# Kernel tuning notes

Measured on AMD Instinct MI355X. Metric: run time of the kernel, lower is better.

Reference implementation:

```python
import jax, jax.numpy as jnp
import numpy as np

B, N, NID, V, GH, PHI, RHO = 8, 256, 64, 128, 128, 256, 128
BN = B * N
EPS = 1e-5


def _layernorm(x, g, b):
    m = jnp.mean(x, axis=-1, keepdims=True)
    v = jnp.var(x, axis=-1, keepdims=True)
    return (x - m) * jax.lax.rsqrt(v + EPS) * g + b


def _edges(A):
    # dense adjacency -> flat batched edge list, exactly as mask.nonzero() ordering
    bidx = jnp.arange(B)[:, None, None]
    ii = jnp.arange(N)[None, :, None]
    jj = jnp.arange(N)[None, None, :]
    src = jnp.broadcast_to(bidx * N + ii, (B, N, N)).reshape(-1)  # edge_index[0] = b*N+i
    tgt = jnp.broadcast_to(bidx * N + jj, (B, N, N)).reshape(-1)  # edge_index[1] = b*N+j
    w = A.reshape(-1)
    valid = w != 0
    rel = (w > 0).astype(jnp.int32)
    return src, tgt, w, valid, rel


def _rgcn(H, src, tgt, valid, rel, Wrel, Wroot, bias):
    # torch_geometric RGCNConv: mean aggregation per relation at target + root + bias
    x_src = H[src]  # (E, d) gather
    out = H @ Wroot + bias
    for r in range(2):
        m = (valid & (rel == r)).astype(H.dtype)  # (E,)
        s = jax.ops.segment_sum(x_src * m[:, None], tgt, num_segments=BN)
        c = jax.ops.segment_sum(m, tgt, num_segments=BN)
        out = out + (s / jnp.maximum(c, 1.0)[:, None]) @ Wrel[r]
    return out


def setup_inputs() -> dict:
    key = jax.random.key(0)
    ks = jax.random.split(key, 24)
    p = lambda k, shape: jax.random.normal(k, shape, dtype=jnp.float32) * 0.02
    z = lambda *shape: jnp.zeros(shape, jnp.float32)
    return {
        "A": jax.random.normal(ks[0], (B, N, N), dtype=jnp.float32),
        "X": jax.random.normal(ks[1], (B, N, NID), dtype=jnp.float32),
        "home_mask": (jax.random.uniform(ks[2], (B, N)) > 0.5).astype(jnp.float32),
        "emb1_w": p(ks[3], (NID, V)), "emb1_b": z(V),
        "emb2_w": p(ks[4], (V, V)), "emb2_b": z(V),
        "rgcn_w_0": p(ks[5], (2, V, GH)), "rgcn_root_0": p(ks[6], (V, GH)), "rgcn_bias_0": z(GH),
        "lina_w_0": p(ks[7], (GH, GH)), "lina_b_0": z(GH),
        "linb_w_0": p(ks[8], (GH, GH)), "linb_b_0": z(GH),
        "rgcn_w_1": p(ks[9], (2, GH, GH)), "rgcn_root_1": p(ks[10], (GH, GH)), "rgcn_bias_1": z(GH),
        "lina_w_1": p(ks[11], (GH, GH)), "lina_b_1": z(GH),
        "linb_w_1": p(ks[12], (GH, GH)), "linb_b_1": z(GH),
        "norm_g": jnp.ones((GH,), jnp.float32), "norm_b": z(GH),
        "phi_w1": p(ks[13], (GH, PHI)), "phi_b1": z(PHI),
        "phi_w2": p(ks[14], (PHI, PHI)), "phi_b2": z(PHI),
        "rho_w1": p(ks[15], (PHI, RHO)), "rho_b1": z(RHO),
        "rho_w2": p(ks[16], (RHO, 1)), "rho_b2": z(1),
    }


def reference(A, X, home_mask, emb1_w, emb1_b, emb2_w, emb2_b,
              rgcn_w_0, rgcn_root_0, rgcn_bias_0, lina_w_0, lina_b_0, linb_w_0, linb_b_0,
              rgcn_w_1, rgcn_root_1, rgcn_bias_1, lina_w_1, lina_b_1, linb_w_1, linb_b_1,
              norm_g, norm_b, phi_w1, phi_b1, phi_w2, phi_b2,
              rho_w1, rho_b1, rho_w2, rho_b2):
    away_mask = 1.0 - home_mask
    H = jax.nn.relu(X @ emb1_w + emb1_b)
    H = (H @ emb2_w + emb2_b).reshape(BN, V)

    src, tgt, w, valid, rel = _edges(A)
    aw = jnp.abs(w) * valid.astype(w.dtype)  # |edge_weight|, zero for masked-out edges

    blocks = [
        (rgcn_w_0, rgcn_root_0, rgcn_bias_0, lina_w_0, lina_b_0, linb_w_0, linb_b_0),
        (rgcn_w_1, rgcn_root_1, rgcn_bias_1, lina_w_1, lina_b_1, linb_w_1, linb_b_1),
    ]
    agg = jnp.zeros_like(H)
    for (Wrel, Wroot, bias, law, lab, lbw, lbb) in blocks:
        H = H + agg
        H2 = _rgcn(H, src, tgt, valid, rel, Wrel, Wroot, bias)
        # gather-scale-scatter: agg[src] += H2[tgt] * |w|
        agg = jax.ops.segment_sum(H2[tgt] * aw[:, None], src, num_segments=BN)
        agg = jax.nn.relu(_layernorm(agg, norm_g, norm_b))  # dropout = identity (eval)
        agg = jax.nn.relu(agg @ law + lab)
        agg = agg @ lbw + lbb
    H = (H + agg).reshape(B, N, GH)

    # DeepSet phi (dropout = identity)
    h = jax.nn.relu(H @ phi_w1 + phi_b1)
    phi_out = jax.nn.relu(h @ phi_w2 + phi_b2)  # (B, N, PHI)

    home_sum = jnp.sum(phi_out * home_mask[:, :, None], axis=1)
    away_sum = jnp.sum(phi_out * away_mask[:, :, None], axis=1)

    def rho(s):
        return (jax.nn.relu(s @ rho_w1 + rho_b1) @ rho_w2 + rho_b2)[:, 0]

    out = rho(home_sum) - rho(away_sum)
    return 0.5 + 0.5 * jnp.tanh(out)  # (B,)
```

## Files before the change

kernel.cpp:

```cpp
#include <hip/hip_runtime.h>
#include <math.h>

#define NB 8


__global__ __launch_bounds__(512, 2) void k_embed(const float* __restrict__ X,
        const float* __restrict__ w1, const float* __restrict__ b1,
        const float* __restrict__ w2, const float* __restrict__ b2,
        float* __restrict__ H, float* __restrict__ pools) {
    const int r0 = blockIdx.x * 8;
    const int t = threadIdx.x, q = t & 31, u = t >> 5, w = t >> 6;
    __shared__ __align__(16) float part[8192];
    __shared__ __align__(16) float xq[512];
    __shared__ __align__(16) float h1q[1024];
    if (blockIdx.x < 8) pools[blockIdx.x * 512 + t] = 0.f;
    {
        int r = t >> 6, k = t & 63;
        xq[k * 8 + r] = X[(size_t)(r0 + r) * 64 + k];
    }
    __syncthreads();
    {
        float acc[32];
        #pragma unroll
        for (int i = 0; i < 32; ++i) acc[i] = 0.f;
        #pragma unroll
        for (int kk = 0; kk < 4; ++kk) {
            int k = u * 4 + kk;
            float4 w4 = *(const float4*)&w1[(size_t)k * 128 + q * 4];
            float wc[4] = {w4.x, w4.y, w4.z, w4.w};
            float4 xa = *(const float4*)&xq[k * 8];
            float4 xb = *(const float4*)&xq[k * 8 + 4];
            float xr[8] = {xa.x, xa.y, xa.z, xa.w, xb.x, xb.y, xb.z, xb.w};
            #pragma unroll
            for (int r = 0; r < 8; ++r)
                #pragma unroll
                for (int c = 0; c < 4; ++c)
                    acc[r * 4 + c] = fmaf(xr[r], wc[c], acc[r * 4 + c]);
        }
        #pragma unroll
        for (int i = 0; i < 32; ++i) acc[i] += __shfl_down(acc[i], 32, 64);
        if ((t & 63) < 32)
            #pragma unroll
            for (int r = 0; r < 8; ++r)
                *(float4*)&part[w * 1024 + r * 128 + q * 4] =
                    make_float4(acc[r*4+0], acc[r*4+1], acc[r*4+2], acc[r*4+3]);
    }
    __syncthreads();
    #pragma unroll
    for (int e = 0; e < 2; ++e) {
        int idx = e * 512 + t;
        int r = idx >> 7, f = idx & 127;
        float s = b1[f];
        #pragma unroll
        for (int uu = 0; uu < 8; ++uu) s += part[uu * 1024 + r * 128 + f];
        h1q[f * 8 + r] = fmaxf(s, 0.f);
    }
    __syncthreads();
    {
        float acc[32];
        #pragma unroll
        for (int i = 0; i < 32; ++i) acc[i] = 0.f;
        #pragma unroll
        for (int kk = 0; kk < 8; ++kk) {
            int k = u * 8 + kk;
            float4 w4 = *(const float4*)&w2[(size_t)k * 128 + q * 4];
            float wc[4] = {w4.x, w4.y, w4.z, w4.w};
            float4 xa = *(const float4*)&h1q[k * 8];
            float4 xb = *(const float4*)&h1q[k * 8 + 4];
            float xr[8] = {xa.x, xa.y, xa.z, xa.w, xb.x, xb.y, xb.z, xb.w};
            #pragma unroll
            for (int r = 0; r < 8; ++r)
                #pragma unroll
                for (int c = 0; c < 4; ++c)
                    acc[r * 4 + c] = fmaf(xr[r], wc[c], acc[r * 4 + c]);
        }
        #pragma unroll
        for (int i = 0; i < 32; ++i) acc[i] += __shfl_down(acc[i], 32, 64);
        if ((t & 63) < 32)
            #pragma unroll
            for (int r = 0; r < 8; ++r)
                *(float4*)&part[w * 1024 + r * 128 + q * 4] =
                    make_float4(acc[r*4+0], acc[r*4+1], acc[r*4+2], acc[r*4+3]);
    }
    __syncthreads();
    #pragma unroll
    for (int e = 0; e < 2; ++e) {
        int idx = e * 512 + t;
        int r = idx >> 7, f = idx & 127;
        float s = b2[f];
        #pragma unroll
        for (int uu = 0; uu < 8; ++uu) s += part[uu * 1024 + r * 128 + f];
        H[(size_t)(r0 + r) * 128 + f] = s;
    }
}

__global__ __launch_bounds__(512, 2) void k_gcn1(
        const float* __restrict__ A, const float* __restrict__ H,
        const float* __restrict__ Wrel, const float* __restrict__ Wroot,
        const float* __restrict__ bias, float* __restrict__ H2) {
    const int b  = blockIdx.x >> 5;
    const int j0 = (blockIdx.x & 31) * 8;
    const int t = threadIdx.x, q = t & 31, u = t >> 5, w = t >> 6;
    __shared__ __align__(16) float maskM[4096];
    __shared__ __align__(16) float part[8192];
    __shared__ __align__(16) float pb[3072];
    __shared__ float cntp[512];
    __shared__ float cnt[16];
    const float* Ab = A + (size_t)b * 65536;
    const float* Hb = H + (size_t)b * 32768;
    const float* W0 = Wrel;
    const float* W1 = Wrel + 16384;

    if (t < 256) {
        float4 a0 = *(const float4*)(Ab + (size_t)t * 256 + j0);
        float4 a1 = *(const float4*)(Ab + (size_t)t * 256 + j0 + 4);
        float av[8] = {a0.x, a0.y, a0.z, a0.w, a1.x, a1.y, a1.z, a1.w};
        #pragma unroll
        for (int j = 0; j < 8; ++j) {
            maskM[t * 16 + j]     = (av[j] < 0.f) ? 1.f : 0.f;
            maskM[t * 16 + 8 + j] = (av[j] > 0.f) ? 1.f : 0.f;
        }
    }
    __syncthreads();
    {
        int chunk = t >> 4, slot = t & 15;
        float c = 0.f;
        #pragma unroll
        for (int qq = 0; qq < 8; ++qq) c += maskM[(chunk * 8 + qq) * 16 + slot];
        cntp[slot * 32 + chunk] = c;
    }
    __syncthreads();
    if (t < 16) {
        float s = 0.f;
        #pragma unroll
        for (int c = 0; c < 32; ++c) s += cntp[t * 32 + c];
        cnt[t] = s;
    }
    {
        float acc[32];
        #pragma unroll
        for (int i = 0; i < 32; ++i) acc[i] = 0.f;
        #pragma unroll 8
        for (int ii = 0; ii < 16; ++ii) {
            int i = u * 16 + ii;
            float4 h4 = *(const float4*)&Hb[(size_t)i * 128 + q * 4];
            float hc[4] = {h4.x, h4.y, h4.z, h4.w};
            float4 ma = *(const float4*)&maskM[i * 16];
            float4 mb = *(const float4*)&maskM[i * 16 + 4];
            float mr[8] = {ma.x, ma.y, ma.z, ma.w, mb.x, mb.y, mb.z, mb.w};
            #pragma unroll
            for (int r = 0; r < 8; ++r)
                #pragma unroll
                for (int c = 0; c < 4; ++c)
                    acc[r * 4 + c] = fmaf(mr[r], hc[c], acc[r * 4 + c]);
        }
        #pragma unroll
        for (int i = 0; i < 32; ++i) acc[i] += __shfl_down(acc[i], 32, 64);
        if ((t & 63) < 32)
            #pragma unroll
            for (int r = 0; r < 8; ++r)
                *(float4*)&part[w * 1024 + r * 128 + q * 4] =
                    make_float4(acc[r*4+0], acc[r*4+1], acc[r*4+2], acc[r*4+3]);
    }
    __syncthreads();
    #pragma unroll
    for (int e = 0; e < 2; ++e) {
        int idx = e * 512 + t;
        int r = idx >> 7, f = idx & 127;
        float s = 0.f;
        #pragma unroll
        for (int uu = 0; uu < 8; ++uu) s += part[uu * 1024 + r * 128 + f];
        pb[f * 24 + 8 + r] = s * (1.f / fmaxf(cnt[r], 1.f));
    }
    __syncthreads();
    {
        float acc[32];
        #pragma unroll
        for (int i = 0; i < 32; ++i) acc[i] = 0.f;
        #pragma unroll 8
        for (int ii = 0; ii < 16; ++ii) {
            int i = u * 16 + ii;
            float4 h4 = *(const float4*)&Hb[(size_t)i * 128 + q * 4];
            float hc[4] = {h4.x, h4.y, h4.z, h4.w};
            float4 ma = *(const float4*)&maskM[i * 16 + 8];
            float4 mb = *(const float4*)&maskM[i * 16 + 12];
            float mr[8] = {ma.x, ma.y, ma.z, ma.w, mb.x, mb.y, mb.z, mb.w};
            #pragma unroll
            for (int r = 0; r < 8; ++r)
                #pragma unroll
                for (int c = 0; c < 4; ++c)
                    acc[r * 4 + c] = fmaf(mr[r], hc[c], acc[r * 4 + c]);
        }
        #pragma unroll
        for (int i = 0; i < 32; ++i) acc[i] += __shfl_down(acc[i], 32, 64);
        if ((t & 63) < 32)
            #pragma unroll
            for (int r = 0; r < 8; ++r)
                *(float4*)&part[w * 1024 + r * 128 + q * 4] =
                    make_float4(acc[r*4+0], acc[r*4+1], acc[r*4+2], acc[r*4+3]);
    }
    __syncthreads();
    #pragma unroll
    for (int e = 0; e < 2; ++e) {
        int idx = e * 512 + t;
        int r = idx >> 7, f = idx & 127;
        float s = 0.f;
        #pragma unroll
        for (int uu = 0; uu < 8; ++uu) s += part[uu * 1024 + r * 128 + f];
        pb[f * 24 + 16 + r] = s * (1.f / fmaxf(cnt[8 + r], 1.f));
        pb[f * 24 + r] = Hb[(size_t)(j0 + r) * 128 + f];
    }
    __syncthreads();
    {
        float acc[32];
        #pragma unroll
        for (int i = 0; i < 32; ++i) acc[i] = 0.f;
        #pragma unroll 4
        for (int kk = 0; kk < 8; ++kk) {
            int k = u * 8 + kk;
            float4 wr = *(const float4*)&Wroot[(size_t)k * 128 + q * 4];
            float4 wa = *(const float4*)&W0[(size_t)k * 128 + q * 4];
            float4 wb = *(const float4*)&W1[(size_t)k * 128 + q * 4];
            float wrc[4] = {wr.x, wr.y, wr.z, wr.w};
            float wac[4] = {wa.x, wa.y, wa.z, wa.w};
            float wbc[4] = {wb.x, wb.y, wb.z, wb.w};
            float4 h0 = *(const float4*)&pb[k * 24];
            float4 h1 = *(const float4*)&pb[k * 24 + 4];
            float4 p0 = *(const float4*)&pb[k * 24 + 8];
            float4 p1 = *(const float4*)&pb[k * 24 + 12];
            float4 q0 = *(const float4*)&pb[k * 24 + 16];
            float4 q1 = *(const float4*)&pb[k * 24 + 20];
            float hr[8]  = {h0.x, h0.y, h0.z, h0.w, h1.x, h1.y, h1.z, h1.w};
            float m0r[8] = {p0.x, p0.y, p0.z, p0.w, p1.x, p1.y, p1.z, p1.w};
            float m1r[8] = {q0.x, q0.y, q0.z, q0.w, q1.x, q1.y, q1.z, q1.w};
            #pragma unroll
            for (int r = 0; r < 8; ++r)
                #pragma unroll
                for (int c = 0; c < 4; ++c) {
                    float v = acc[r * 4 + c];
                    v = fmaf(hr[r],  wrc[c], v);
                    v = fmaf(m0r[r], wac[c], v);
                    v = fmaf(m1r[r], wbc[c], v);
                    acc[r * 4 + c] = v;
                }
        }
        #pragma unroll
        for (int i = 0; i < 32; ++i) acc[i] += __shfl_down(acc[i], 32, 64);
        if ((t & 63) < 32)
            #pragma unroll
            for (int r = 0; r < 8; ++r)
                *(float4*)&part[w * 1024 + r * 128 + q * 4] =
                    make_float4(acc[r*4+0], acc[r*4+1], acc[r*4+2], acc[r*4+3]);
    }
    __syncthreads();
    #pragma unroll
    for (int e = 0; e < 2; ++e) {
        int idx = e * 512 + t;
        int r = idx >> 7, f = idx & 127;
        float s = bias[f];
        #pragma unroll
        for (int uu = 0; uu < 8; ++uu) s += part[uu * 1024 + r * 128 + f];
        H2[(size_t)(b * 256 + j0 + r) * 128 + f] = s;
    }
}

__global__ __launch_bounds__(512, 2) void k_gcn2(
        const float* __restrict__ A, const float* __restrict__ H2,
        const float* __restrict__ g, const float* __restrict__ bta,
        const float* __restrict__ law, const float* __restrict__ lab,
        const float* __restrict__ lbw, const float* __restrict__ lbb,
        float* __restrict__ H) {
    const int b  = blockIdx.x >> 5;
    const int i0 = (blockIdx.x & 31) * 8;
    const int t = threadIdx.x, q = t & 31, u = t >> 5, w = t >> 6;
    __shared__ __align__(16) float part[8192];
    __shared__ __align__(16) float absA[2048];
    __shared__ __align__(16) float xq[1024];
    __shared__ __align__(16) float uq[1024];
    __shared__ float red[32];
    __shared__ float mi[16];
    const float* Ab  = A + (size_t)b * 65536;
    const float* H2b = H2 + (size_t)b * 32768;

    if (t < 256) {
        #pragma unroll
        for (int r = 0; r < 8; ++r)
            absA[t * 8 + r] = fabsf(Ab[(size_t)(i0 + r) * 256 + t]);
    }
    __syncthreads();
    {
        float acc[32];
        #pragma unroll
        for (int i = 0; i < 32; ++i) acc[i] = 0.f;
        #pragma unroll 8
        for (int jj = 0; jj < 16; ++jj) {
            int j = u * 16 + jj;
            float4 h4 = *(const float4*)&H2b[(size_t)j * 128 + q * 4];
            float hc[4] = {h4.x, h4.y, h4.z, h4.w};
            float4 aa = *(const float4*)&absA[j * 8];
            float4 ab = *(const float4*)&absA[j * 8 + 4];
            float ar[8] = {aa.x, aa.y, aa.z, aa.w, ab.x, ab.y, ab.z, ab.w};
            #pragma unroll
            for (int r = 0; r < 8; ++r)
                #pragma unroll
                for (int c = 0; c < 4; ++c)
                    acc[r * 4 + c] = fmaf(ar[r], hc[c], acc[r * 4 + c]);
        }
        #pragma unroll
        for (int i = 0; i < 32; ++i) acc[i] += __shfl_down(acc[i], 32, 64);
        if ((t & 63) < 32)
            #pragma unroll
            for (int r = 0; r < 8; ++r)
                *(float4*)&part[w * 1024 + r * 128 + q * 4] =
                    make_float4(acc[r*4+0], acc[r*4+1], acc[r*4+2], acc[r*4+3]);
    }
    __syncthreads();
    float xv[2];
    const int fof = t & 127;
    #pragma unroll
    for (int e = 0; e < 2; ++e) {
        int idx = e * 512 + t;
        int r = idx >> 7;
        float s = 0.f;
        #pragma unroll
        for (int uu = 0; uu < 8; ++uu) s += part[uu * 1024 + r * 128 + fof];
        xv[e] = s;
        float sw = s, s2 = s * s;
        #pragma unroll
        for (int o = 32; o > 0; o >>= 1) {
            sw += __shfl_down(sw, o, 64);
            s2 += __shfl_down(s2, o, 64);
        }
        if ((t & 63) == 0) {
            int half = (t >> 6) & 1;
            red[r * 4 + half * 2]     = sw;
            red[r * 4 + half * 2 + 1] = s2;
        }
    }
    __syncthreads();
    if (t < 8) {
        float s  = red[t * 4]     + red[t * 4 + 2];
        float s2 = red[t * 4 + 1] + red[t * 4 + 3];
        float m = s * (1.f / 128.f);
        float v = s2 * (1.f / 128.f) - m * m;
        mi[t * 2] = m;
        mi[t * 2 + 1] = rsqrtf(v + 1e-5f);
    }
    __syncthreads();
    {
        float gf = g[fof], bf = bta[fof];
        #pragma unroll
        for (int e = 0; e < 2; ++e) {
            int r = ((e * 512 + t) >> 7);
            xq[fof * 8 + r] = fmaxf((xv[e] - mi[r * 2]) * mi[r * 2 + 1] * gf + bf, 0.f);
        }
    }
    __syncthreads();
    {
        float acc[32];
        #pragma unroll
        for (int i = 0; i < 32; ++i) acc[i] = 0.f;
        #pragma unroll
        for (int kk = 0; kk < 8; ++kk) {
            int k = u * 8 + kk;
            float4 w4 = *(const float4*)&law[(size_t)k * 128 + q * 4];
            float wc[4] = {w4.x, w4.y, w4.z, w4.w};
            float4 xa = *(const float4*)&xq[k * 8];
            float4 xb = *(const float4*)&xq[k * 8 + 4];
            float xr[8] = {xa.x, xa.y, xa.z, xa.w, xb.x, xb.y, xb.z, xb.w};
            #pragma unroll
            for (int r = 0; r < 8; ++r)
                #pragma unroll
                for (int c = 0; c < 4; ++c)
                    acc[r * 4 + c] = fmaf(xr[r], wc[c], acc[r * 4 + c]);
        }
        #pragma unroll
        for (int i = 0; i < 32; ++i) acc[i] += __shfl_down(acc[i], 32, 64);
        if ((t & 63) < 32)
            #pragma unroll
            for (int r = 0; r < 8; ++r)
                *(float4*)&part[w * 1024 + r * 128 + q * 4] =
                    make_float4(acc[r*4+0], acc[r*4+1], acc[r*4+2], acc[r*4+3]);
    }
    __syncthreads();
    #pragma unroll
    for (int e = 0; e < 2; ++e) {
        int idx = e * 512 + t;
        int r = idx >> 7, f = idx & 127;
        float s = lab[f];
        #pragma unroll
        for (int uu = 0; uu < 8; ++uu) s += part[uu * 1024 + r * 128 + f];
        uq[f * 8 + r] = fmaxf(s, 0.f);
    }
    __syncthreads();
    {
        float acc[32];
        #pragma unroll
        for (int i = 0; i < 32; ++i) acc[i] = 0.f;
        #pragma unroll
        for (int kk = 0; kk < 8; ++kk) {
            int k = u * 8 + kk;
            float4 w4 = *(const float4*)&lbw[(size_t)k * 128 + q * 4];
            float wc[4] = {w4.x, w4.y, w4.z, w4.w};
            float4 xa = *(const float4*)&uq[k * 8];
            float4 xb = *(const float4*)&uq[k * 8 + 4];
            float xr[8] = {xa.x, xa.y, xa.z, xa.w, xb.x, xb.y, xb.z, xb.w};
            #pragma unroll
            for (int r = 0; r < 8; ++r)
                #pragma unroll
                for (int c = 0; c < 4; ++c)
                    acc[r * 4 + c] = fmaf(xr[r], wc[c], acc[r * 4 + c]);
        }
        #pragma unroll
        for (int i = 0; i < 32; ++i) acc[i] += __shfl_down(acc[i], 32, 64);
        if ((t & 63) < 32)
            #pragma unroll
            for (int r = 0; r < 8; ++r)
                *(float4*)&part[w * 1024 + r * 128 + q * 4] =
                    make_float4(acc[r*4+0], acc[r*4+1], acc[r*4+2], acc[r*4+3]);
    }
    __syncthreads();
    #pragma unroll
    for (int e = 0; e < 2; ++e) {
        int idx = e * 512 + t;
        int r = idx >> 7, f = idx & 127;
        float s = lbb[f];
        #pragma unroll
        for (int uu = 0; uu < 8; ++uu) s += part[uu * 1024 + r * 128 + f];
        size_t hidx = (size_t)(b * 256 + i0 + r) * 128 + f;
        H[hidx] = s + H[hidx];
    }
}

__global__ __launch_bounds__(512, 2) void k_deepset(
        const float* __restrict__ H, const float* __restrict__ hm,
        const float* __restrict__ w1, const float* __restrict__ b1,
        const float* __restrict__ w2, const float* __restrict__ b2,
        float* __restrict__ hsum, float* __restrict__ asum) {
    const int r0 = blockIdx.x * 8;
    const int b  = blockIdx.x >> 5;
    const int t  = threadIdx.x, q = t & 63, u = t >> 6;
    __shared__ __align__(16) float part[8192];
    __shared__ __align__(16) float ph2[2048];
    __shared__ __align__(16) float hraw[1024];
    __shared__ float hmv[8];
    #pragma unroll
    for (int e = 0; e < 2; ++e) {
        int idx = e * 512 + t;
        int r = idx >> 7, k = idx & 127;
        hraw[k * 8 + r] = H[(size_t)(r0 + r) * 128 + k];
    }
    if (t < 8) hmv[t] = hm[r0 + t];
    __syncthreads();
    float acc[32];
    #pragma unroll
    for (int i = 0; i < 32; ++i) acc[i] = 0.f;
    #pragma unroll 8
    for (int kk = 0; kk < 16; ++kk) {
        int k = u * 16 + kk;
        float4 w4 = *(const float4*)&w1[(size_t)k * 256 + q * 4];
        float wc[4] = {w4.x, w4.y, w4.z, w4.w};
        float4 ha = *(const float4*)&hraw[k * 8];
        float4 hb = *(const float4*)&hraw[k * 8 + 4];
        float hr[8] = {ha.x, ha.y, ha.z, ha.w, hb.x, hb.y, hb.z, hb.w};
        #pragma unroll
        for (int r = 0; r < 8; ++r)
            #pragma unroll
            for (int c = 0; c < 4; ++c)
                acc[r * 4 + c] = fmaf(hr[r], wc[c], acc[r * 4 + c]);
    }
    #pragma unroll
    for (int pass = 0; pass < 2; ++pass) {
        #pragma unroll
        for (int r = 0; r < 4; ++r)
            *(float4*)&part[u * 1024 + r * 256 + q * 4] =
                make_float4(acc[(pass*4+r)*4+0], acc[(pass*4+r)*4+1],
                            acc[(pass*4+r)*4+2], acc[(pass*4+r)*4+3]);
        __syncthreads();
        #pragma unroll
        for (int e = 0; e < 2; ++e) {
            int idx = e * 512 + t;
            int r = idx >> 8, f = idx & 255;
            float s = b1[f];
            #pragma unroll
            for (int uu = 0; uu < 8; ++uu) s += part[uu * 1024 + r * 256 + f];
            ph2[f * 8 + pass * 4 + r] = fmaxf(s, 0.f);
        }
        __syncthreads();
    }
    float a2[32];
    #pragma unroll
    for (int i = 0; i < 32; ++i) a2[i] = 0.f;
    #pragma unroll 8
    for (int kk = 0; kk < 32; ++kk) {
        int k = u * 32 + kk;
        float4 w4 = *(const float4*)&w2[(size_t)k * 256 + q * 4];
        float wc[4] = {w4.x, w4.y, w4.z, w4.w};
        float4 pa = *(const float4*)&ph2[k * 8];
        float4 pbv = *(const float4*)&ph2[k * 8 + 4];
        float pr[8] = {pa.x, pa.y, pa.z, pa.w, pbv.x, pbv.y, pbv.z, pbv.w};
        #pragma unroll
        for (int r = 0; r < 8; ++r)
            #pragma unroll
            for (int c = 0; c < 4; ++c)
                a2[r * 4 + c] = fmaf(pr[r], wc[c], a2[r * 4 + c]);
    }
    __syncthreads();
    #pragma unroll
    for (int pass = 0; pass < 2; ++pass) {
        #pragma unroll
        for (int r = 0; r < 4; ++r)
            *(float4*)&part[u * 1024 + r * 256 + q * 4] =
                make_float4(a2[(pass*4+r)*4+0], a2[(pass*4+r)*4+1],
                            a2[(pass*4+r)*4+2], a2[(pass*4+r)*4+3]);
        __syncthreads();
        #pragma unroll
        for (int e = 0; e < 2; ++e) {
            int idx = e * 512 + t;
            int r = idx >> 8, f = idx & 255;
            float s = 0.f;
            #pragma unroll
            for (int uu = 0; uu < 8; ++uu) s += part[uu * 1024 + r * 256 + f];
            ph2[f * 8 + pass * 4 + r] = s;
        }
        __syncthreads();
    }
    if (t < 256) {
        float bb = b2[t];
        float hp = 0.f, sp = 0.f;
        #pragma unroll
        for (int r = 0; r < 8; ++r) {
            float p = fmaxf(ph2[t * 8 + r] + bb, 0.f);
            sp += p;
            hp = fmaf(p, hmv[r], hp);
        }
        atomicAdd(&hsum[b * 256 + t], hp);
        atomicAdd(&asum[b * 256 + t], sp - hp);
    }
}

__global__ __launch_bounds__(256) void k_rho(const float* __restrict__ hsum,
        const float* __restrict__ asum,
        const float* __restrict__ w1, const float* __restrict__ b1,
        const float* __restrict__ w2, const float* __restrict__ b2,
        float* __restrict__ out) {
    const int bIdx = blockIdx.x;
// ... 55 lines not shown
    const float* rgcn_bias[2] = { (const float*)d_in[9],  (const float*)d_in[16] };
    const float* lina_w[2]    = { (const float*)d_in[10], (const float*)d_in[17] };
    const float* lina_b[2]    = { (const float*)d_in[11], (const float*)d_in[18] };
    const float* linb_w[2]    = { (const float*)d_in[12], (const float*)d_in[19] };
    const float* linb_b[2]    = { (const float*)d_in[13], (const float*)d_in[20] };
    const float* norm_g  = (const float*)d_in[21];
    const float* norm_b  = (const float*)d_in[22];
    const float* phi_w1  = (const float*)d_in[23];
    const float* phi_b1  = (const float*)d_in[24];
    const float* phi_w2  = (const float*)d_in[25];
    const float* phi_b2  = (const float*)d_in[26];
    const float* rho_w1  = (const float*)d_in[27];
    const float* rho_b1  = (const float*)d_in[28];
    const float* rho_w2  = (const float*)d_in[29];
    const float* rho_b2  = (const float*)d_in[30];
    float* out = (float*)d_out;

    float* ws   = (float*)d_ws;
    float* H    = ws;
    float* H2   = ws + 262144;
    float* hsum = ws + 524288;
    float* asum = ws + 526336;

    k_embed<<<256, 512, 0, stream>>>(X, emb1_w, emb1_b, emb2_w, emb2_b, H, hsum);

    for (int it = 0; it < 2; ++it) {
        k_gcn1<<<256, 512, 0, stream>>>(A, H, rgcn_w[it], rgcn_root[it],
                                        rgcn_bias[it], H2);
        k_gcn2<<<256, 512, 0, stream>>>(A, H2, norm_g, norm_b,
                                        lina_w[it], lina_b[it],
                                        linb_w[it], linb_b[it], H);
    }

    k_deepset<<<256, 512, 0, stream>>>(H, home_mask, phi_w1, phi_b1,
                                       phi_w2, phi_b2, hsum, asum);
    k_rho<<<NB, 256, 0, stream>>>(hsum, asum, rho_w1, rho_b1, rho_w2, rho_b2, out);
}
```

Measured before the change: 206.5 us.

## Double threads per block and split row tiles across half-wavefronts

```diff
diff --git a/kernel.cpp b/kernel.cpp
--- a/kernel.cpp
+++ b/kernel.cpp
@@ -4,103 +4,95 @@
 #define NB 8
 
 
-__global__ __launch_bounds__(512, 2) void k_embed(const float* __restrict__ X,
+__global__ __launch_bounds__(1024, 4) void k_embed(const float* __restrict__ X,
         const float* __restrict__ w1, const float* __restrict__ b1,
         const float* __restrict__ w2, const float* __restrict__ b2,
         float* __restrict__ H, float* __restrict__ pools) {
     const int r0 = blockIdx.x * 8;
-    const int t = threadIdx.x, q = t & 31, u = t >> 5, w = t >> 6;
+    const int t = threadIdx.x, q = t & 31, h = (t >> 5) & 1, u = t >> 6;
     __shared__ __align__(16) float part[8192];
     __shared__ __align__(16) float xq[512];
     __shared__ __align__(16) float h1q[1024];
-    if (blockIdx.x < 8) pools[blockIdx.x * 512 + t] = 0.f;
-    {
+    if (blockIdx.x < 4) pools[blockIdx.x * 1024 + t] = 0.f;
+    if (t < 512) {
         int r = t >> 6, k = t & 63;
         xq[k * 8 + r] = X[(size_t)(r0 + r) * 64 + k];
     }
     __syncthreads();
-    {
-        float acc[32];
-        #pragma unroll
-        for (int i = 0; i < 32; ++i) acc[i] = 0.f;
-        #pragma unroll
-        for (int kk = 0; kk < 4; ++kk) {
-            int k = u * 4 + kk;
-            float4 w4 = *(const float4*)&w1[(size_t)k * 128 + q * 4];
-            float wc[4] = {w4.x, w4.y, w4.z, w4.w};
-            float4 xa = *(const float4*)&xq[k * 8];
-            float4 xb = *(const float4*)&xq[k * 8 + 4];
-            float xr[8] = {xa.x, xa.y, xa.z, xa.w, xb.x, xb.y, xb.z, xb.w};
-            #pragma unroll
-            for (int r = 0; r < 8; ++r)
-                #pragma unroll
-                for (int c = 0; c < 4; ++c)
-                    acc[r * 4 + c] = fmaf(xr[r], wc[c], acc[r * 4 + c]);
-        }
-        #pragma unroll
-        for (int i = 0; i < 32; ++i) acc[i] += __shfl_down(acc[i], 32, 64);
-        if ((t & 63) < 32)
-            #pragma unroll
-            for (int r = 0; r < 8; ++r)
-                *(float4*)&part[w * 1024 + r * 128 + q * 4] =
-                    make_float4(acc[r*4+0], acc[r*4+1], acc[r*4+2], acc[r*4+3]);
-    }
-    __syncthreads();
-    #pragma unroll
-    for (int e = 0; e < 2; ++e) {
-        int idx = e * 512 + t;
-        int r = idx >> 7, f = idx & 127;
-        float s = b1[f];
-        #pragma unroll
-        for (int uu = 0; uu < 8; ++uu) s += part[uu * 1024 + r * 128 + f];
-        h1q[f * 8 + r] = fmaxf(s, 0.f);
-    }
-    __syncthreads();
-    {
-        float acc[32];
-        #pragma unroll
-        for (int i = 0; i < 32; ++i) acc[i] = 0.f;
-        #pragma unroll
-        for (int kk = 0; kk < 8; ++kk) {
-            int k = u * 8 + kk;
-            float4 w4 = *(const float4*)&w2[(size_t)k * 128 + q * 4];
-            float wc[4] = {w4.x, w4.y, w4.z, w4.w};
-            float4 xa = *(const float4*)&h1q[k * 8];
-            float4 xb = *(const float4*)&h1q[k * 8 + 4];
-            float xr[8] = {xa.x, xa.y, xa.z, xa.w, xb.x, xb.y, xb.z, xb.w};
-            #pragma unroll
-            for (int r = 0; r < 8; ++r)
-                #pragma unroll
-                for (int c = 0; c < 4; ++c)
-                    acc[r * 4 + c] = fmaf(xr[r], wc[c], acc[r * 4 + c]);
-        }
-        #pragma unroll
-        for (int i = 0; i < 32; ++i) acc[i] += __shfl_down(acc[i], 32, 64);
-        if ((t & 63) < 32)
-            #pragma unroll
-            for (int r = 0; r < 8; ++r)
-                *(float4*)&part[w * 1024 + r * 128 + q * 4] =
-                    make_float4(acc[r*4+0], acc[r*4+1], acc[r*4+2], acc[r*4+3]);
-    }
-    __syncthreads();
-    #pragma unroll
-    for (int e = 0; e < 2; ++e) {
-        int idx = e * 512 + t;
-        int r = idx >> 7, f = idx & 127;
-        float s = b2[f];
-        #pragma unroll
-        for (int uu = 0; uu < 8; ++uu) s += part[uu * 1024 + r * 128 + f];
-        H[(size_t)(r0 + r) * 128 + f] = s;
+    float acc[16];
+    #pragma unroll
+    for (int i = 0; i < 16; ++i) acc[i] = 0.f;
+    #pragma unroll
+    for (int kk = 0; kk < 4; ++kk) {
+        int k = u * 4 + kk;
+        float4 w4 = *(const float4*)&w1[(size_t)k * 128 + q * 4];
+        float wc[4] = {w4.x, w4.y, w4.z, w4.w};
+        float4 x4 = *(const float4*)&xq[k * 8 + h * 4];
+        float xr[4] = {x4.x, x4.y, x4.z, x4.w};
+        #pragma unroll
+        for (int r = 0; r < 4; ++r)
+            #pragma unroll
+            for (int c = 0; c < 4; ++c)
+                acc[r * 4 + c] = fmaf(xr[r], wc[c], acc[r * 4 + c]);
+    }
+    #pragma unroll
+    for (int p = 0; p < 2; ++p) {
+        if (h == p)
+            #pragma unroll
+            for (int r = 0; r < 4; ++r)
+                *(float4*)&part[u * 512 + r * 128 + q * 4] =
+                    make_float4(acc[r*4+0], acc[r*4+1], acc[r*4+2], acc[r*4+3]);
+        __syncthreads();
+        if (t < 512) {
+            int r = t >> 7, f = t & 127, row = p * 4 + r;
+            float s = b1[f];
+            #pragma unroll
+            for (int uu = 0; uu < 16; ++uu) s += part[uu * 512 + r * 128 + f];
+            h1q[f * 8 + row] = fmaxf(s, 0.f);
+        }
+        __syncthreads();
+    }
+    #pragma unroll
+    for (int i = 0; i < 16; ++i) acc[i] = 0.f;
+    #pragma unroll
+    for (int kk = 0; kk < 8; ++kk) {
+        int k = u * 8 + kk;
+        float4 w4 = *(const float4*)&w2[(size_t)k * 128 + q * 4];
+        float wc[4] = {w4.x, w4.y, w4.z, w4.w};
+        float4 x4 = *(const float4*)&h1q[k * 8 + h * 4];
+        float xr[4] = {x4.x, x4.y, x4.z, x4.w};
+        #pragma unroll
+        for (int r = 0; r < 4; ++r)
+            #pragma unroll
+            for (int c = 0; c < 4; ++c)
+                acc[r * 4 + c] = fmaf(xr[r], wc[c], acc[r * 4 + c]);
+    }
+    #pragma unroll
+    for (int p = 0; p < 2; ++p) {
+        if (h == p)
+            #pragma unroll
+            for (int r = 0; r < 4; ++r)
+                *(float4*)&part[u * 512 + r * 128 + q * 4] =
+                    make_float4(acc[r*4+0], acc[r*4+1], acc[r*4+2], acc[r*4+3]);
+        __syncthreads();
+        if (t < 512) {
+            int r = t >> 7, f = t & 127, row = p * 4 + r;
+            float s = b2[f];
+            #pragma unroll
+            for (int uu = 0; uu < 16; ++uu) s += part[uu * 512 + r * 128 + f];
+            H[(size_t)(r0 + row) * 128 + f] = s;
+        }
+        __syncthreads();
     }
 }
 
-__global__ __launch_bounds__(512, 2) void k_gcn1(
+__global__ __launch_bounds__(1024, 4) void k_gcn1(
         const float* __restrict__ A, const float* __restrict__ H,
         const float* __restrict__ Wrel, const float* __restrict__ Wroot,
         const float* __restrict__ bias, float* __restrict__ H2) {
     const int b  = blockIdx.x >> 5;
     const int j0 = (blockIdx.x & 31) * 8;
-    const int t = threadIdx.x, q = t & 31, u = t >> 5, w = t >> 6;
+    const int t = threadIdx.x, q = t & 31, h = (t >> 5) & 1, u = t >> 6;
     __shared__ __align__(16) float maskM[4096];
     __shared__ __align__(16) float part[8192];
     __shared__ __align__(16) float pb[3072];
@@ -122,7 +114,7 @@
         }
     }
     __syncthreads();
-    {
+    if (t < 512) {
         int chunk = t >> 4, slot = t & 15;
         float c = 0.f;
         #pragma unroll
@@ -136,135 +128,123 @@
         for (int c = 0; c < 32; ++c) s += cntp[t * 32 + c];
         cnt[t] = s;
     }
-    {
-        float acc[32];
-        #pragma unroll
-        for (int i = 0; i < 32; ++i) acc[i] = 0.f;
-        #pragma unroll 8
-        for (int ii = 0; ii < 16; ++ii) {
-            int i = u * 16 + ii;
-            float4 h4 = *(const float4*)&Hb[(size_t)i * 128 + q * 4];
-            float hc[4] = {h4.x, h4.y, h4.z, h4.w};
-            float4 ma = *(const float4*)&maskM[i * 16];
-            float4 mb = *(const float4*)&maskM[i * 16 + 4];
-            float mr[8] = {ma.x, ma.y, ma.z, ma.w, mb.x, mb.y, mb.z, mb.w};
-            #pragma unroll
-            for (int r = 0; r < 8; ++r)
-                #pragma unroll
-                for (int c = 0; c < 4; ++c)
-                    acc[r * 4 + c] = fmaf(mr[r], hc[c], acc[r * 4 + c]);
-        }
-        #pragma unroll
-        for (int i = 0; i < 32; ++i) acc[i] += __shfl_down(acc[i], 32, 64);
-        if ((t & 63) < 32)
-            #pragma unroll
-            for (int r = 0; r < 8; ++r)
-                *(float4*)&part[w * 1024 + r * 128 + q * 4] =
-                    make_float4(acc[r*4+0], acc[r*4+1], acc[r*4+2], acc[r*4+3]);
-    }
-    __syncthreads();
-    #pragma unroll
-    for (int e = 0; e < 2; ++e) {
-        int idx = e * 512 + t;
-        int r = idx >> 7, f = idx & 127;
-        float s = 0.f;
-        #pragma unroll
-        for (int uu = 0; uu < 8; ++uu) s += part[uu * 1024 + r * 128 + f];
-        pb[f * 24 + 8 + r] = s * (1.f / fmaxf(cnt[r], 1.f));
-    }
-    __syncthreads();
-    {
-        float acc[32];
-        #pragma unroll
-        for (int i = 0; i < 32; ++i) acc[i] = 0.f;
-        #pragma unroll 8
-        for (int ii = 0; ii < 16; ++ii) {
-            int i = u * 16 + ii;
-            float4 h4 = *(const float4*)&Hb[(size_t)i * 128 + q * 4];
-            float hc[4] = {h4.x, h4.y, h4.z, h4.w};
-            float4 ma = *(const float4*)&maskM[i * 16 + 8];
-            float4 mb = *(const float4*)&maskM[i * 16 + 12];
-            float mr[8] = {ma.x, ma.y, ma.z, ma.w, mb.x, mb.y, mb.z, mb.w};
-            #pragma unroll
-            for (int r = 0; r < 8; ++r)
-                #pragma unroll
-                for (int c = 0; c < 4; ++c)
-                    acc[r * 4 + c] = fmaf(mr[r], hc[c], acc[r * 4 + c]);
-        }
-        #pragma unroll
-        for (int i = 0; i < 32; ++i) acc[i] += __shfl_down(acc[i], 32, 64);
-        if ((t & 63) < 32)
-            #pragma unroll
-            for (int r = 0; r < 8; ++r)
-                *(float4*)&part[w * 1024 + r * 128 + q * 4] =
-                    make_float4(acc[r*4+0], acc[r*4+1], acc[r*4+2], acc[r*4+3]);
-    }
-    __syncthreads();
-    #pragma unroll
-    for (int e = 0; e < 2; ++e) {
-        int idx = e * 512 + t;
-        int r = idx >> 7, f = idx & 127;
-        float s = 0.f;
-        #pragma unroll
-        for (int uu = 0; uu < 8; ++uu) s += part[uu * 1024 + r * 128 + f];
-        pb[f * 24 + 16 + r] = s * (1.f / fmaxf(cnt[8 + r], 1.f));
-        pb[f * 24 + r] = Hb[(size_t)(j0 + r) * 128 + f];
-    }
-    __syncthreads();
-    {
-        float acc[32];
-        #pragma unroll
-        for (int i = 0; i < 32; ++i) acc[i] = 0.f;
-        #pragma unroll 4
-        for (int kk = 0; kk < 8; ++kk) {
-            int k = u * 8 + kk;
-            float4 wr = *(const float4*)&Wroot[(size_t)k * 128 + q * 4];
-            float4 wa = *(const float4*)&W0[(size_t)k * 128 + q * 4];
-            float4 wb = *(const float4*)&W1[(size_t)k * 128 + q * 4];
-            float wrc[4] = {wr.x, wr.y, wr.z, wr.w};
-            float wac[4] = {wa.x, wa.y, wa.z, wa.w};
-            float wbc[4] = {wb.x, wb.y, wb.z, wb.w};
-            float4 h0 = *(const float4*)&pb[k * 24];
-            float4 h1 = *(const float4*)&pb[k * 24 + 4];
-            float4 p0 = *(const float4*)&pb[k * 24 + 8];
-            float4 p1 = *(const float4*)&pb[k * 24 + 12];
-            float4 q0 = *(const float4*)&pb[k * 24 + 16];
-            float4 q1 = *(const float4*)&pb[k * 24 + 20];
-            float hr[8]  = {h0.x, h0.y, h0.z, h0.w, h1.x, h1.y, h1.z, h1.w};
-            float m0r[8] = {p0.x, p0.y, p0.z, p0.w, p1.x, p1.y, p1.z, p1.w};
-            float m1r[8] = {q0.x, q0.y, q0.z, q0.w, q1.x, q1.y, q1.z, q1.w};
-            #pragma unroll
-            for (int r = 0; r < 8; ++r)
-                #pragma unroll
-                for (int c = 0; c < 4; ++c) {
-                    float v = acc[r * 4 + c];
-                    v = fmaf(hr[r],  wrc[c], v);
-                    v = fmaf(m0r[r], wac[c], v);
-                    v = fmaf(m1r[r], wbc[c], v);
-                    acc[r * 4 + c] = v;
-                }
-        }
-        #pragma unroll
-        for (int i = 0; i < 32; ++i) acc[i] += __shfl_down(acc[i], 32, 64);
-        if ((t & 63) < 32)
-            #pragma unroll
-            for (int r = 0; r < 8; ++r)
-                *(float4*)&part[w * 1024 + r * 128 + q * 4] =
-                    make_float4(acc[r*4+0], acc[r*4+1], acc[r*4+2], acc[r*4+3]);
-    }
-    __syncthreads();
-    #pragma unroll
-    for (int e = 0; e < 2; ++e) {
-        int idx = e * 512 + t;
-        int r = idx >> 7, f = idx & 127;
-        float s = bias[f];
-        #pragma unroll
-        for (int uu = 0; uu < 8; ++uu) s += part[uu * 1024 + r * 128 + f];
-        H2[(size_t)(b * 256 + j0 + r) * 128 + f] = s;
+    float acc[16];
+    #pragma unroll
+    for (int i = 0; i < 16; ++i) acc[i] = 0.f;
+    #pragma unroll 8
+    for (int ii = 0; ii < 16; ++ii) {
+        int i = u * 16 + ii;
+        float4 h4 = *(const float4*)&Hb[(size_t)i * 128 + q * 4];
+        float hc[4] = {h4.x, h4.y, h4.z, h4.w};
+        float4 m4 = *(const float4*)&maskM[i * 16 + h * 4];
+        float mr[4] = {m4.x, m4.y, m4.z, m4.w};
+        #pragma unroll
+        for (int r = 0; r < 4; ++r)
+            #pragma unroll
+            for (int c = 0; c < 4; ++c)
+                acc[r * 4 + c] = fmaf(mr[r], hc[c], acc[r * 4 + c]);
+    }
+    #pragma unroll
+    for (int p = 0; p < 2; ++p) {
+        if (h == p)
+            #pragma unroll
+            for (int r = 0; r < 4; ++r)
+                *(float4*)&part[u * 512 + r * 128 + q * 4] =
+                    make_float4(acc[r*4+0], acc[r*4+1], acc[r*4+2], acc[r*4+3]);
+        __syncthreads();
+        if (t < 512) {
+            int r = t >> 7, f = t & 127, row = p * 4 + r;
+            float s = 0.f;
+            #pragma unroll
+            for (int uu = 0; uu < 16; ++uu) s += part[uu * 512 + r * 128 + f];
+            pb[f * 24 + 8 + row] = s * (1.f / fmaxf(cnt[row], 1.f));
+        }
+        __syncthreads();
+    }
+    #pragma unroll
+    for (int i = 0; i < 16; ++i) acc[i] = 0.f;
+    #pragma unroll 8
+    for (int ii = 0; ii < 16; ++ii) {
+        int i = u * 16 + ii;
+        float4 h4 = *(const float4*)&Hb[(size_t)i * 128 + q * 4];
+        float hc[4] = {h4.x, h4.y, h4.z, h4.w};
+        float4 m4 = *(const float4*)&maskM[i * 16 + 8 + h * 4];
+        float mr[4] = {m4.x, m4.y, m4.z, m4.w};
+        #pragma unroll
+        for (int r = 0; r < 4; ++r)
+            #pragma unroll
+            for (int c = 0; c < 4; ++c)
+                acc[r * 4 + c] = fmaf(mr[r], hc[c], acc[r * 4 + c]);
+    }
+    #pragma unroll
+    for (int p = 0; p < 2; ++p) {
+        if (h == p)
+            #pragma unroll
+            for (int r = 0; r < 4; ++r)
+                *(float4*)&part[u * 512 + r * 128 + q * 4] =
+                    make_float4(acc[r*4+0], acc[r*4+1], acc[r*4+2], acc[r*4+3]);
+        __syncthreads();
+        if (t < 512) {
+            int r = t >> 7, f = t & 127, row = p * 4 + r;
+            float s = 0.f;
+            #pragma unroll
+            for (int uu = 0; uu < 16; ++uu) s += part[uu * 512 + r * 128 + f];
+            pb[f * 24 + 16 + row] = s * (1.f / fmaxf(cnt[8 + row], 1.f));
+        } else {
+            int idx = p * 512 + (t - 512);
+            int r8 = idx >> 7, f2 = idx & 127;
+            pb[f2 * 24 + r8] = Hb[(size_t)(j0 + r8) * 128 + f2];
+        }
+        __syncthreads();
+    }
+    #pragma unroll
+    for (int i = 0; i < 16; ++i) acc[i] = 0.f;
+    #pragma unroll
+    for (int kk = 0; kk < 8; ++kk) {
+        int k = u * 8 + kk;
+        float4 wr = *(const float4*)&Wroot[(size_t)k * 128 + q * 4];
+        float4 wa = *(const float4*)&W0[(size_t)k * 128 + q * 4];
+        float4 wb = *(const float4*)&W1[(size_t)k * 128 + q * 4];
+        float wrc[4] = {wr.x, wr.y, wr.z, wr.w};
+        float wac[4] = {wa.x, wa.y, wa.z, wa.w};
+        float wbc[4] = {wb.x, wb.y, wb.z, wb.w};
+        float4 hv = *(const float4*)&pb[k * 24 + h * 4];
+        float4 p0 = *(const float4*)&pb[k * 24 + 8 + h * 4];
+        float4 p1 = *(const float4*)&pb[k * 24 + 16 + h * 4];
+        float hr[4]  = {hv.x, hv.y, hv.z, hv.w};
+        float m0r[4] = {p0.x, p0.y, p0.z, p0.w};
+        float m1r[4] = {p1.x, p1.y, p1.z, p1.w};
+        #pragma unroll
+        for (int r = 0; r < 4; ++r)
+            #pragma unroll
+            for (int c = 0; c < 4; ++c) {
+                float v = acc[r * 4 + c];
+                v = fmaf(hr[r],  wrc[c], v);
+                v = fmaf(m0r[r], wac[c], v);
+                v = fmaf(m1r[r], wbc[c], v);
+                acc[r * 4 + c] = v;
+            }
+    }
+    #pragma unroll
+    for (int p = 0; p < 2; ++p) {
+        if (h == p)
+            #pragma unroll
+            for (int r = 0; r < 4; ++r)
+                *(float4*)&part[u * 512 + r * 128 + q * 4] =
+                    make_float4(acc[r*4+0], acc[r*4+1], acc[r*4+2], acc[r*4+3]);
+        __syncthreads();
+        if (t < 512) {
+            int r = t >> 7, f = t & 127, row = p * 4 + r;
+            float s = bias[f];
+            #pragma unroll
+            for (int uu = 0; uu < 16; ++uu) s += part[uu * 512 + r * 128 + f];
+            H2[(size_t)(b * 256 + j0 + row) * 128 + f] = s;
+        }
+        __syncthreads();
     }
 }
 
-__global__ __launch_bounds__(512, 2) void k_gcn2(
+__global__ __launch_bounds__(1024, 4) void k_gcn2(
         const float* __restrict__ A, const float* __restrict__ H2,
         const float* __restrict__ g, const float* __restrict__ bta,
         const float* __restrict__ law, const float* __restrict__ lab,
@@ -272,7 +252,7 @@
         float* __restrict__ H) {
     const int b  = blockIdx.x >> 5;
     const int i0 = (blockIdx.x & 31) * 8;
-    const int t = threadIdx.x, q = t & 31, u = t >> 5, w = t >> 6;
+    const int t = threadIdx.x, q = t & 31, h = (t >> 5) & 1, u = t >> 6;
     __shared__ __align__(16) float part[8192];
     __shared__ __align__(16) float absA[2048];
     __shared__ __align__(16) float xq[1024];
@@ -288,44 +268,43 @@
             absA[t * 8 + r] = fabsf(Ab[(size_t)(i0 + r) * 256 + t]);
     }
     __syncthreads();
+    float acc[16];
+    #pragma unroll
+    for (int i = 0; i < 16; ++i) acc[i] = 0.f;
+    #pragma unroll 8
+    for (int jj = 0; jj < 16; ++jj) {
+        int j = u * 16 + jj;
+        float4 h4 = *(const float4*)&H2b[(size_t)j * 128 + q * 4];
+        float hc[4] = {h4.x, h4.y, h4.z, h4.w};
+        float4 a4 = *(const float4*)&absA[j * 8 + h * 4];
+        float ar[4] = {a4.x, a4.y, a4.z, a4.w};
+        #pragma unroll
+        for (int r = 0; r < 4; ++r)
+            #pragma unroll
+            for (int c = 0; c < 4; ++c)
+                acc[r * 4 + c] = fmaf(ar[r], hc[c], acc[r * 4 + c]);
+    }
+    #pragma unroll
+    for (int p = 0; p < 2; ++p) {
+        if (h == p)
+            #pragma unroll
+            for (int r = 0; r < 4; ++r)
+                *(float4*)&part[u * 512 + r * 128 + q * 4] =
+                    make_float4(acc[r*4+0], acc[r*4+1], acc[r*4+2], acc[r*4+3]);
+        __syncthreads();
+        if (t < 512) {
+            int r = t >> 7, f = t & 127, row = p * 4 + r;
+            float s = 0.f;
+            #pragma unroll
+            for (int uu = 0; uu < 16; ++uu) s += part[uu * 512 + r * 128 + f];
+            xq[f * 8 + row] = s;
+        }
+        __syncthreads();
+    }
     {
-        float acc[32];
-        #pragma unroll
-        for (int i = 0; i < 32; ++i) acc[i] = 0.f;
-        #pragma unroll 8
-        for (int jj = 0; jj < 16; ++jj) {
-            int j = u * 16 + jj;
-            float4 h4 = *(const float4*)&H2b[(size_t)j * 128 + q * 4];
-            float hc[4] = {h4.x, h4.y, h4.z, h4.w};
-            float4 aa = *(const float4*)&absA[j * 8];
-            float4 ab = *(const float4*)&absA[j * 8 + 4];
-            float ar[8] = {aa.x, aa.y, aa.z, aa.w, ab.x, ab.y, ab.z, ab.w};
-            #pragma unroll
-            for (int r = 0; r < 8; ++r)
-                #pragma unroll
-                for (int c = 0; c < 4; ++c)
-                    acc[r * 4 + c] = fmaf(ar[r], hc[c], acc[r * 4 + c]);
-        }
-        #pragma unroll
-        for (int i = 0; i < 32; ++i) acc[i] += __shfl_down(acc[i], 32, 64);
-        if ((t & 63) < 32)
-            #pragma unroll
-            for (int r = 0; r < 8; ++r)
-                *(float4*)&part[w * 1024 + r * 128 + q * 4] =
-                    make_float4(acc[r*4+0], acc[r*4+1], acc[r*4+2], acc[r*4+3]);
-    }
-    __syncthreads();
-    float xv[2];
-    const int fof = t & 127;
-    #pragma unroll
-    for (int e = 0; e < 2; ++e) {
-        int idx = e * 512 + t;
-        int r = idx >> 7;
-        float s = 0.f;
-        #pragma unroll
-        for (int uu = 0; uu < 8; ++uu) s += part[uu * 1024 + r * 128 + fof];
-        xv[e] = s;
-        float sw = s, s2 = s * s;
+        int r = t >> 7, f = t & 127;
+        float x = xq[f * 8 + r];
+        float sw = x, s2 = x * x;
         #pragma unroll
         for (int o = 32; o > 0; o >>= 1) {
             sw += __shfl_down(sw, o, 64);
@@ -336,192 +315,167 @@
             red[r * 4 + half * 2]     = sw;
             red[r * 4 + half * 2 + 1] = s2;
         }
-    }
-    __syncthreads();
-    if (t < 8) {
-        float s  = red[t * 4]     + red[t * 4 + 2];
-        float s2 = red[t * 4 + 1] + red[t * 4 + 3];
-        float m = s * (1.f / 128.f);
-        float v = s2 * (1.f / 128.f) - m * m;
-        mi[t * 2] = m;
-        mi[t * 2 + 1] = rsqrtf(v + 1e-5f);
-    }
-    __syncthreads();
-    {
-        float gf = g[fof], bf = bta[fof];
-        #pragma unroll
-        for (int e = 0; e < 2; ++e) {
-            int r = ((e * 512 + t) >> 7);
-            xq[fof * 8 + r] = fmaxf((xv[e] - mi[r * 2]) * mi[r * 2 + 1] * gf + bf, 0.f);
-        }
-    }
-    __syncthreads();
-    {
-        float acc[32];
-        #pragma unroll
-        for (int i = 0; i < 32; ++i) acc[i] = 0.f;
-        #pragma unroll
-        for (int kk = 0; kk < 8; ++kk) {
-            int k = u * 8 + kk;
-            float4 w4 = *(const float4*)&law[(size_t)k * 128 + q * 4];
-            float wc[4] = {w4.x, w4.y, w4.z, w4.w};
-            float4 xa = *(const float4*)&xq[k * 8];
-            float4 xb = *(const float4*)&xq[k * 8 + 4];
-            float xr[8] = {xa.x, xa.y, xa.z, xa.w, xb.x, xb.y, xb.z, xb.w};
-            #pragma unroll
-            for (int r = 0; r < 8; ++r)
-                #pragma unroll
-                for (int c = 0; c < 4; ++c)
-                    acc[r * 4 + c] = fmaf(xr[r], wc[c], acc[r * 4 + c]);
-        }
-        #pragma unroll
-        for (int i = 0; i < 32; ++i) acc[i] += __shfl_down(acc[i], 32, 64);
-        if ((t & 63) < 32)
-            #pragma unroll
-            for (int r = 0; r < 8; ++r)
-                *(float4*)&part[w * 1024 + r * 128 + q * 4] =
-                    make_float4(acc[r*4+0], acc[r*4+1], acc[r*4+2], acc[r*4+3]);
-    }
-    __syncthreads();
-    #pragma unroll
-    for (int e = 0; e < 2; ++e) {
-        int idx = e * 512 + t;
-        int r = idx >> 7, f = idx & 127;
-        float s = lab[f];
-        #pragma unroll
-        for (int uu = 0; uu < 8; ++uu) s += part[uu * 1024 + r * 128 + f];
-        uq[f * 8 + r] = fmaxf(s, 0.f);
-    }
-    __syncthreads();
-    {
-        float acc[32];
-        #pragma unroll
-        for (int i = 0; i < 32; ++i) acc[i] = 0.f;
-        #pragma unroll
-        for (int kk = 0; kk < 8; ++kk) {
-            int k = u * 8 + kk;
-            float4 w4 = *(const float4*)&lbw[(size_t)k * 128 + q * 4];
-            float wc[4] = {w4.x, w4.y, w4.z, w4.w};
-            float4 xa = *(const float4*)&uq[k * 8];
-            float4 xb = *(const float4*)&uq[k * 8 + 4];
-            float xr[8] = {xa.x, xa.y, xa.z, xa.w, xb.x, xb.y, xb.z, xb.w};
-            #pragma unroll
-            for (int r = 0; r < 8; ++r)
-                #pragma unroll
-                for (int c = 0; c < 4; ++c)
-                    acc[r * 4 + c] = fmaf(xr[r], wc[c], acc[r * 4 + c]);
-        }
-        #pragma unroll
-        for (int i = 0; i < 32; ++i) acc[i] += __shfl_down(acc[i], 32, 64);
-        if ((t & 63) < 32)
-            #pragma unroll
-            for (int r = 0; r < 8; ++r)
-                *(float4*)&part[w * 1024 + r * 128 + q * 4] =
-                    make_float4(acc[r*4+0], acc[r*4+1], acc[r*4+2], acc[r*4+3]);
-    }
-    __syncthreads();
-    #pragma unroll
-    for (int e = 0; e < 2; ++e) {
-        int idx = e * 512 + t;
-        int r = idx >> 7, f = idx & 127;
-        float s = lbb[f];
-        #pragma unroll
-        for (int uu = 0; uu < 8; ++uu) s += part[uu * 1024 + r * 128 + f];
-        size_t hidx = (size_t)(b * 256 + i0 + r) * 128 + f;
-        H[hidx] = s + H[hidx];
+        __syncthreads();
+        if (t < 8) {
+            float s  = red[t * 4]     + red[t * 4 + 2];
+            float ss = red[t * 4 + 1] + red[t * 4 + 3];
+            float m = s * (1.f / 128.f);
+            float v = ss * (1.f / 128.f) - m * m;
+            mi[t * 2] = m;
+            mi[t * 2 + 1] = rsqrtf(v + 1e-5f);
+        }
+        __syncthreads();
+        xq[f * 8 + r] = fmaxf((x - mi[r * 2]) * mi[r * 2 + 1] * g[f] + bta[f], 0.f);
+    }
+    __syncthreads();
+    #pragma unroll
+    for (int i = 0; i < 16; ++i) acc[i] = 0.f;
+    #pragma unroll
+    for (int kk = 0; kk < 8; ++kk) {
+        int k = u * 8 + kk;
+        float4 w4 = *(const float4*)&law[(size_t)k * 128 + q * 4];
+        float wc[4] = {w4.x, w4.y, w4.z, w4.w};
+        float4 x4 = *(const float4*)&xq[k * 8 + h * 4];
+        float xr[4] = {x4.x, x4.y, x4.z, x4.w};
+        #pragma unroll
+        for (int r = 0; r < 4; ++r)
+            #pragma unroll
+            for (int c = 0; c < 4; ++c)
+                acc[r * 4 + c] = fmaf(xr[r], wc[c], acc[r * 4 + c]);
+    }
+    #pragma unroll
+    for (int p = 0; p < 2; ++p) {
+        if (h == p)
+            #pragma unroll
+            for (int r = 0; r < 4; ++r)
+                *(float4*)&part[u * 512 + r * 128 + q * 4] =
+                    make_float4(acc[r*4+0], acc[r*4+1], acc[r*4+2], acc[r*4+3]);
+        __syncthreads();
+        if (t < 512) {
+            int r = t >> 7, f = t & 127, row = p * 4 + r;
+            float s = lab[f];
+            #pragma unroll
+            for (int uu = 0; uu < 16; ++uu) s += part[uu * 512 + r * 128 + f];
+            uq[f * 8 + row] = fmaxf(s, 0.f);
+        }
+        __syncthreads();
+    }
+    #pragma unroll
+    for (int i = 0; i < 16; ++i) acc[i] = 0.f;
+    #pragma unroll
+    for (int kk = 0; kk < 8; ++kk) {
+        int k = u * 8 + kk;
+        float4 w4 = *(const float4*)&lbw[(size_t)k * 128 + q * 4];
+        float wc[4] = {w4.x, w4.y, w4.z, w4.w};
+        float4 x4 = *(const float4*)&uq[k * 8 + h * 4];
+        float xr[4] = {x4.x, x4.y, x4.z, x4.w};
+        #pragma unroll
+        for (int r = 0; r < 4; ++r)
+            #pragma unroll
+            for (int c = 0; c < 4; ++c)
+                acc[r * 4 + c] = fmaf(xr[r], wc[c], acc[r * 4 + c]);
+    }
+    #pragma unroll
+    for (int p = 0; p < 2; ++p) {
+        if (h == p)
+            #pragma unroll
+            for (int r = 0; r < 4; ++r)
+                *(float4*)&part[u * 512 + r * 128 + q * 4] =
+                    make_float4(acc[r*4+0], acc[r*4+1], acc[r*4+2], acc[r*4+3]);
+        __syncthreads();
+        if (t < 512) {
+            int r = t >> 7, f = t & 127, row = p * 4 + r;
+            float s = lbb[f];
+            #pragma unroll
+            for (int uu = 0; uu < 16; ++uu) s += part[uu * 512 + r * 128 + f];
+            size_t idx = (size_t)(b * 256 + i0 + row) * 128 + f;
+            H[idx] = s + H[idx];
+        }
+        __syncthreads();
     }
 }
 
-__global__ __launch_bounds__(512, 2) void k_deepset(
+__global__ __launch_bounds__(1024, 4) void k_deepset(
         const float* __restrict__ H, const float* __restrict__ hm,
         const float* __restrict__ w1, const float* __restrict__ b1,
         const float* __restrict__ w2, const float* __restrict__ b2,
         float* __restrict__ hsum, float* __restrict__ asum) {
     const int r0 = blockIdx.x * 8;
     const int b  = blockIdx.x >> 5;
-    const int t  = threadIdx.x, q = t & 63, u = t >> 6;
+    const int t  = threadIdx.x, q = t & 63, hw = (t >> 6) & 1, u = t >> 7;
     __shared__ __align__(16) float part[8192];
     __shared__ __align__(16) float ph2[2048];
     __shared__ __align__(16) float hraw[1024];
     __shared__ float hmv[8];
-    #pragma unroll
-    for (int e = 0; e < 2; ++e) {
-        int idx = e * 512 + t;
-        int r = idx >> 7, k = idx & 127;
+    {
+        int r = t >> 7, k = t & 127;
         hraw[k * 8 + r] = H[(size_t)(r0 + r) * 128 + k];
     }
     if (t < 8) hmv[t] = hm[r0 + t];
     __syncthreads();
-    float acc[32];
-    #pragma unroll
-    for (int i = 0; i < 32; ++i) acc[i] = 0.f;
+    float acc[16];
+    #pragma unroll
+    for (int i = 0; i < 16; ++i) acc[i] = 0.f;
     #pragma unroll 8
     for (int kk = 0; kk < 16; ++kk) {
         int k = u * 16 + kk;
         float4 w4 = *(const float4*)&w1[(size_t)k * 256 + q * 4];
         float wc[4] = {w4.x, w4.y, w4.z, w4.w};
-        float4 ha = *(const float4*)&hraw[k * 8];
-        float4 hb = *(const float4*)&hraw[k * 8 + 4];
-        float hr[8] = {ha.x, ha.y, ha.z, ha.w, hb.x, hb.y, hb.z, hb.w};
-        #pragma unroll
-        for (int r = 0; r < 8; ++r)
+        float4 h4 = *(const float4*)&hraw[k * 8 + hw * 4];
+        float hr[4] = {h4.x, h4.y, h4.z, h4.w};
+        #pragma unroll
+        for (int r = 0; r < 4; ++r)
             #pragma unroll
             for (int c = 0; c < 4; ++c)
                 acc[r * 4 + c] = fmaf(hr[r], wc[c], acc[r * 4 + c]);
     }
     #pragma unroll
-    for (int pass = 0; pass < 2; ++pass) {
-        #pragma unroll
-        for (int r = 0; r < 4; ++r)
-            *(float4*)&part[u * 1024 + r * 256 + q * 4] =
-                make_float4(acc[(pass*4+r)*4+0], acc[(pass*4+r)*4+1],
-                            acc[(pass*4+r)*4+2], acc[(pass*4+r)*4+3]);
-        __syncthreads();
-        #pragma unroll
-        for (int e = 0; e < 2; ++e) {
-            int idx = e * 512 + t;
-            int r = idx >> 8, f = idx & 255;
+    for (int p = 0; p < 2; ++p) {
+        if (hw == p)
+            #pragma unroll
+            for (int r = 0; r < 4; ++r)
+                *(float4*)&part[u * 1024 + r * 256 + q * 4] =
+                    make_float4(acc[r*4+0], acc[r*4+1], acc[r*4+2], acc[r*4+3]);
+        __syncthreads();
+        {
+            int r = t >> 8, f = t & 255, row = p * 4 + r;
             float s = b1[f];
             #pragma unroll
             for (int uu = 0; uu < 8; ++uu) s += part[uu * 1024 + r * 256 + f];
-            ph2[f * 8 + pass * 4 + r] = fmaxf(s, 0.f);
-        }
-        __syncthreads();
-    }
-    float a2[32];
-    #pragma unroll
-    for (int i = 0; i < 32; ++i) a2[i] = 0.f;
+            ph2[f * 8 + row] = fmaxf(s, 0.f);
+        }
+        __syncthreads();
+    }
+    #pragma unroll
+    for (int i = 0; i < 16; ++i) acc[i] = 0.f;
     #pragma unroll 8
     for (int kk = 0; kk < 32; ++kk) {
         int k = u * 32 + kk;
         float4 w4 = *(const float4*)&w2[(size_t)k * 256 + q * 4];
         float wc[4] = {w4.x, w4.y, w4.z, w4.w};
-        float4 pa = *(const float4*)&ph2[k * 8];
-        float4 pbv = *(const float4*)&ph2[k * 8 + 4];
-        float pr[8] = {pa.x, pa.y, pa.z, pa.w, pbv.x, pbv.y, pbv.z, pbv.w};
-        #pragma unroll
-        for (int r = 0; r < 8; ++r)
-            #pragma unroll
-            for (int c = 0; c < 4; ++c)
-                a2[r * 4 + c] = fmaf(pr[r], wc[c], a2[r * 4 + c]);
-    }
-    __syncthreads();
-    #pragma unroll
-    for (int pass = 0; pass < 2; ++pass) {
-        #pragma unroll
-        for (int r = 0; r < 4; ++r)
-            *(float4*)&part[u * 1024 + r * 256 + q * 4] =
-                make_float4(a2[(pass*4+r)*4+0], a2[(pass*4+r)*4+1],
-                            a2[(pass*4+r)*4+2], a2[(pass*4+r)*4+3]);
-        __syncthreads();
-        #pragma unroll
-        for (int e = 0; e < 2; ++e) {
-            int idx = e * 512 + t;
-            int r = idx >> 8, f = idx & 255;
+        float4 p4 = *(const float4*)&ph2[k * 8 + hw * 4];
+        float pr[4] = {p4.x, p4.y, p4.z, p4.w};
+        #pragma unroll
+        for (int r = 0; r < 4; ++r)
+            #pragma unroll
+            for (int c = 0; c < 4; ++c)
+                acc[r * 4 + c] = fmaf(pr[r], wc[c], acc[r * 4 + c]);
+    }
+    __syncthreads();
+    #pragma unroll
+    for (int p = 0; p < 2; ++p) {
+        if (hw == p)
+            #pragma unroll
+            for (int r = 0; r < 4; ++r)
+                *(float4*)&part[u * 1024 + r * 256 + q * 4] =
+                    make_float4(acc[r*4+0], acc[r*4+1], acc[r*4+2], acc[r*4+3]);
+        __syncthreads();
+        {
+            int r = t >> 8, f = t & 255, row = p * 4 + r;
             float s = 0.f;
             #pragma unroll
             for (int uu = 0; uu < 8; ++uu) s += part[uu * 1024 + r * 256 + f];
-            ph2[f * 8 + pass * 4 + r] = s;
+            ph2[f * 8 + row] = s;
         }
         __syncthreads();
     }
@@ -623,17 +577,17 @@
     float* hsum = ws + 524288;
     float* asum = ws + 526336;
 
-    k_embed<<<256, 512, 0, stream>>>(X, emb1_w, emb1_b, emb2_w, emb2_b, H, hsum);
+    k_embed<<<256, 1024, 0, stream>>>(X, emb1_w, emb1_b, emb2_w, emb2_b, H, hsum);
 
     for (int it = 0; it < 2; ++it) {
-        k_gcn1<<<256, 512, 0, stream>>>(A, H, rgcn_w[it], rgcn_root[it],
-                                        rgcn_bias[it], H2);
-        k_gcn2<<<256, 512, 0, stream>>>(A, H2, norm_g, norm_b,
-                                        lina_w[it], lina_b[it],
-                                        linb_w[it], linb_b[it], H);
-    }
-
-    k_deepset<<<256, 512, 0, stream>>>(H, home_mask, phi_w1, phi_b1,
-                                       phi_w2, phi_b2, hsum, asum);
+        k_gcn1<<<256, 1024, 0, stream>>>(A, H, rgcn_w[it], rgcn_root[it],
+                                         rgcn_bias[it], H2);
+        k_gcn2<<<256, 1024, 0, stream>>>(A, H2, norm_g, norm_b,
+                                         lina_w[it], lina_b[it],
+                                         linb_w[it], linb_b[it], H);
+    }
+
+    k_deepset<<<256, 1024, 0, stream>>>(H, home_mask, phi_w1, phi_b1,
+                                        phi_w2, phi_b2, hsum, asum);
     k_rho<<<NB, 256, 0, stream>>>(hsum, asum, rho_w1, rho_b1, rho_w2, rho_b2, out);
 }
```

Result: faster. 197.5 us (-4.4%).
